# Kernel optimization log

Hardware: AMD Instinct MI355X
Metric: run time of the kernel (lower is better)

The kernel has to match this reference:

```python
import jax, jax.numpy as jnp
import numpy as np

N_NODES = 50000
N_EDGES = 625000
FEAT = 128
NEG_SLOPE = 0.2  # dgl GATConv default leaky_relu slope


def setup_inputs() -> dict:
    key = jax.random.key(0)
    ks = jax.random.split(key, 16)
    x = jax.random.normal(ks[0], (N_NODES, FEAT), dtype=jnp.float32)
    src = jax.random.randint(ks[1], (N_EDGES,), 0, N_NODES, dtype=jnp.int32)
    dst = jax.random.randint(ks[2], (N_EDGES,), 0, N_NODES, dtype=jnp.int32)
    s = 1.0 / np.sqrt(FEAT)
    d = {"x": x, "src": src, "dst": dst}
    for i in range(3):
        d[f"W{i+1}"] = jax.random.normal(ks[3 + 4 * i], (FEAT, FEAT), dtype=jnp.float32) * s
        d[f"al{i+1}"] = jax.random.normal(ks[4 + 4 * i], (FEAT,), dtype=jnp.float32) * s
        d[f"ar{i+1}"] = jax.random.normal(ks[5 + 4 * i], (FEAT,), dtype=jnp.float32) * s
        d[f"b{i+1}"] = jnp.zeros((FEAT,), dtype=jnp.float32)
    return d


def gat_layer(h_in, src, dst, W, al, ar, b):
    # dgl GATConv, num_heads=1: fc -> edge attention -> edge_softmax -> scatter
    h = h_in @ W                                   # [N, F]
    el = h @ al                                    # [N]
    er = h @ ar                                    # [N]
    e = jax.nn.leaky_relu(el[src] + er[dst], NEG_SLOPE)   # [E]
    # numerically stable edge softmax, grouped by destination node
    m = jax.ops.segment_max(e, dst, num_segments=N_NODES)  # [N]
    ex = jnp.exp(e - m[dst])
    denom = jax.ops.segment_sum(ex, dst, num_segments=N_NODES)
    alpha = ex / denom[dst]                        # [E]
    out = jax.ops.segment_sum(alpha[:, None] * h[src], dst, num_segments=N_NODES)
    return out + b


def reference(x, src, dst, W1, al1, ar1, b1, W2, al2, ar2, b2, W3, al3, ar3, b3):
    h = gat_layer(x, src, dst, W1, al1, ar1, b1)
    h = jax.nn.relu(h)
    h = gat_layer(h, src, dst, W2, al2, ar2, b2)
    h = jax.nn.relu(h)
    h = gat_layer(h, src, dst, W3, al3, ar3, b3)
    return h
```

## Files before the change

kernel.cpp:

```cpp
#include <hip/hip_runtime.h>
#include <hip/hip_fp16.h>

#define N_NODES 50000
#define N_EDGES 625000
#define FEAT 128
#define NEG_SLOPE 0.2f
#define NB_SCAN 196

typedef __attribute__((ext_vector_type(8))) short bf16x8;
typedef __attribute__((ext_vector_type(4))) float f32x4;

__device__ __forceinline__ unsigned short f2bf(float f) {
  unsigned u = __float_as_uint(f);
  u += 0x7fffu + ((u >> 16) & 1u);
  return (unsigned short)(u >> 16);
}
__device__ __forceinline__ float bf2f(unsigned short s) {
  return __uint_as_float(((unsigned)s) << 16);
}


__global__ __launch_bounds__(256) void prepzero_kernel(
    const float* __restrict__ W0, const float* __restrict__ W1, const float* __restrict__ W2,
    unsigned short* __restrict__ wfhi, unsigned short* __restrict__ wflo,
    int* __restrict__ cnt) {
  int bb = blockIdx.x;
  if (bb < 192) {
    int idx = bb * 256 + threadIdx.x;
    if (idx >= 3 * FEAT * FEAT) return;
    int l = idx >> 14, rem = idx & 16383;
    int e = rem & 7, lane = (rem >> 3) & 63, kb = (rem >> 9) & 3, ct = rem >> 11;
    int col = ct * 16 + (lane & 15);
    int k   = kb * 32 + (lane >> 4) * 8 + e;
    const float* W = (l == 0) ? W0 : ((l == 1) ? W1 : W2);
    float v = W[k * FEAT + col];
    unsigned short hi = f2bf(v);
    wfhi[idx] = hi;
    wflo[idx] = f2bf(v - bf2f(hi));
  } else {
    int i = (bb - 192) * 256 + threadIdx.x;
    if (i < N_NODES + 16) cnt[i] = 0;
  }
}


__global__ __launch_bounds__(256) void hist_kernel(const int* __restrict__ dst,
                                                   int* __restrict__ cnt) {
  int e = blockIdx.x * 256 + threadIdx.x;
  if (e < N_EDGES) atomicAdd(&cnt[dst[e]], 1);
}

__global__ __launch_bounds__(256) void scan_part_kernel(const int* __restrict__ cnt,
                                                        int* __restrict__ part) {
  __shared__ int s[256];
  int i = blockIdx.x * 256 + threadIdx.x;
  s[threadIdx.x] = (i < N_NODES) ? cnt[i] : 0;
  __syncthreads();
  for (int o = 128; o > 0; o >>= 1) {
    if (threadIdx.x < o) s[threadIdx.x] += s[threadIdx.x + o];
    __syncthreads();
  }
  if (threadIdx.x == 0) part[blockIdx.x] = s[0];
}

__global__ __launch_bounds__(256) void scan_top_kernel(int* __restrict__ part,
                                                       int* __restrict__ offs) {
  __shared__ int s[256];
  int tid = threadIdx.x;
  int v = (tid < NB_SCAN) ? part[tid] : 0;
  s[tid] = v;
  __syncthreads();
  for (int o = 1; o < 256; o <<= 1) {
    int t = (tid >= o) ? s[tid - o] : 0;
    __syncthreads();
    s[tid] += t;
    __syncthreads();
  }
  if (tid < NB_SCAN) part[tid] = s[tid] - v;
  if (tid == 255) offs[N_NODES] = s[255];
}

__global__ __launch_bounds__(256) void scan_down_kernel(int* __restrict__ cnt,
                                                        const int* __restrict__ part,
                                                        int* __restrict__ offs) {
  __shared__ int s[256];
  int tid = threadIdx.x;
  int i = blockIdx.x * 256 + tid;
  int v = (i < N_NODES) ? cnt[i] : 0;
  s[tid] = v;
  __syncthreads();
  for (int o = 1; o < 256; o <<= 1) {
    int t = (tid >= o) ? s[tid - o] : 0;
    __syncthreads();
    s[tid] += t;
    __syncthreads();
  }
  if (i < N_NODES) {
    int excl = s[tid] - v + part[blockIdx.x];
    offs[i] = excl;
    cnt[i] = excl;
  }
}

__global__ __launch_bounds__(256) void fill_kernel(const int* __restrict__ src,
                                                   const int* __restrict__ dst,
                                                   int* __restrict__ cursor,
                                                   int* __restrict__ ssrc) {
  int e = blockIdx.x * 256 + threadIdx.x;
  if (e < N_EDGES) {
    int pos = atomicAdd(&cursor[dst[e]], 1);
    ssrc[pos] = src[e];
  }
}


__global__ __launch_bounds__(256) void gemm_mfma_kernel(
    const float* __restrict__ inF, const __half* __restrict__ inH,
    const unsigned short* __restrict__ wfhi, const unsigned short* __restrict__ wflo,
    const float* __restrict__ al, const float* __restrict__ ar,
    __half* __restrict__ h, float* __restrict__ el, float* __restrict__ er,
    int fp16relu_in)
{
  __shared__ unsigned short wl[16384];
  __shared__ __half tile[64][132];
  const int tid = threadIdx.x;
  const int wave = tid >> 6, lane = tid & 63;
  const int lrow = lane & 15, lkb = lane >> 4;
  const int arow_i = blockIdx.x * 64 + wave * 16 + lrow;
  const bool avalid = arow_i < N_NODES;

#pragma unroll
  for (int q = 0; q < 8; ++q) {
    int idx = q * 256 + tid;
    int hilo = idx >> 10, r = idx & 1023, frag = r >> 6, word = r & 63;
    int ct = frag >> 1, kb = frag & 1;
    const uint4* s4 = (const uint4*)(hilo ? wflo : wfhi);
    uint4 v = s4[(ct * 4 + kb) * 64 + word];
    *(uint4*)&wl[((hilo * 16 + frag) << 9) + word * 8] = v;
  }

  bf16x8 ahi[4], alo[4];
#pragma unroll
  for (int kb = 0; kb < 4; ++kb) {
    float a[8];
    if (avalid) {
      if (fp16relu_in) {
        const unsigned short* aH = (const unsigned short*)inH + (size_t)arow_i * FEAT;
        uint4 rv = *(const uint4*)(aH + kb * 32 + lkb * 8);
        const __half2* hp = (const __half2*)&rv;
#pragma unroll
        for (int e2 = 0; e2 < 4; ++e2) {
          float2 f = __half22float2(hp[e2]);
          a[e2 * 2] = fmaxf(f.x, 0.f); a[e2 * 2 + 1] = fmaxf(f.y, 0.f);
        }
      } else {
        const float* arow = inF + (size_t)arow_i * FEAT;
        float4 v0 = *(const float4*)(arow + kb * 32 + lkb * 8);
        float4 v1 = *(const float4*)(arow + kb * 32 + lkb * 8 + 4);
        a[0] = v0.x; a[1] = v0.y; a[2] = v0.z; a[3] = v0.w;
        a[4] = v1.x; a[5] = v1.y; a[6] = v1.z; a[7] = v1.w;
      }
    } else {
#pragma unroll
      for (int e = 0; e < 8; ++e) a[e] = 0.f;
    }
#pragma unroll
    for (int e = 0; e < 8; ++e) {
      unsigned short hb = f2bf(a[e]);
      ahi[kb][e] = (short)hb;
      alo[kb][e] = (short)f2bf(a[e] - bf2f(hb));
    }
  }

  f32x4 acc[8];
#pragma unroll
  for (int ct = 0; ct < 8; ++ct)
#pragma unroll
    for (int r = 0; r < 4; ++r) acc[ct][r] = 0.f;

  __syncthreads();
#pragma unroll
  for (int ct = 0; ct < 8; ++ct) {
#pragma unroll
    for (int kb1 = 0; kb1 < 2; ++kb1) {
      bf16x8 bhi = *(const bf16x8*)&wl[((ct * 2 + kb1) << 9) + lane * 8];
      bf16x8 blo = *(const bf16x8*)&wl[((16 + ct * 2 + kb1) << 9) + lane * 8];
      acc[ct] = __builtin_amdgcn_mfma_f32_16x16x32_bf16(ahi[kb1], bhi, acc[ct], 0, 0, 0);
      acc[ct] = __builtin_amdgcn_mfma_f32_16x16x32_bf16(ahi[kb1], blo, acc[ct], 0, 0, 0);
      acc[ct] = __builtin_amdgcn_mfma_f32_16x16x32_bf16(alo[kb1], bhi, acc[ct], 0, 0, 0);
    }
  }
  __syncthreads();

#pragma unroll
  for (int q = 0; q < 8; ++q) {
    int idx = q * 256 + tid;
    int hilo = idx >> 10, r = idx & 1023, frag = r >> 6, word = r & 63;
    int ct = frag >> 1, kb = 2 + (frag & 1);
    const uint4* s4 = (const uint4*)(hilo ? wflo : wfhi);
    uint4 v = s4[(ct * 4 + kb) * 64 + word];
    *(uint4*)&wl[((hilo * 16 + frag) << 9) + word * 8] = v;
  }
  __syncthreads();
#pragma unroll
  for (int ct = 0; ct < 8; ++ct) {
#pragma unroll
    for (int kb1 = 0; kb1 < 2; ++kb1) {
      bf16x8 bhi = *(const bf16x8*)&wl[((ct * 2 + kb1) << 9) + lane * 8];
      bf16x8 blo = *(const bf16x8*)&wl[((16 + ct * 2 + kb1) << 9) + lane * 8];
      acc[ct] = __builtin_amdgcn_mfma_f32_16x16x32_bf16(ahi[2 + kb1], bhi, acc[ct], 0, 0, 0);
      acc[ct] = __builtin_amdgcn_mfma_f32_16x16x32_bf16(ahi[2 + kb1], blo, acc[ct], 0, 0, 0);
      acc[ct] = __builtin_amdgcn_mfma_f32_16x16x32_bf16(alo[2 + kb1], bhi, acc[ct], 0, 0, 0);
    }
  }

  float alv[8], arv[8];
#pragma unroll
  for (int ct = 0; ct < 8; ++ct) { alv[ct] = al[ct * 16 + lrow]; arv[ct] = ar[ct * 16 + lrow]; }

  const int lrow0 = wave * 16 + lkb * 4;
#pragma unroll
  for (int r = 0; r < 4; ++r) {
    float pel = 0.f, per_ = 0.f;
#pragma unroll
    for (int ct = 0; ct < 8; ++ct) {
      float v = acc[ct][r];
      tile[lrow0 + r][ct * 16 + lrow] = __float2half_rn(v);
      pel  = fmaf(v, alv[ct], pel);
      per_ = fmaf(v, arv[ct], per_);
    }
#pragma unroll
    for (int mask = 8; mask >= 1; mask >>= 1) {
      pel  += __shfl_xor(pel, mask);
      per_ += __shfl_xor(per_, mask);
    }
    int grow = blockIdx.x * 64 + lrow0 + r;
    if (grow < N_NODES && lrow == 0) { el[grow] = pel; er[grow] = per_; }
  }
  __syncthreads();

  const int row0g = blockIdx.x * 64;
#pragma unroll
  for (int it = 0; it < 4; ++it) {
    int idx = it * 256 + tid;
    int row = idx >> 4, c16 = idx & 15;
    int grow = row0g + row;
    if (grow < N_NODES) {
      uint4 v = *(const uint4*)&tile[row][c16 * 8];
      *((uint4*)(h + (size_t)grow * FEAT) + c16) = v;
    }
  }
}


__global__ __launch_bounds__(256) void agg_kernel(
    const __half* __restrict__ h, const float* __restrict__ el,
    const float* __restrict__ er, const int* __restrict__ offs,
    const int* __restrict__ ssrc, const float* __restrict__ bias,
    float* __restrict__ out32, __half* __restrict__ out16, int use16)
{
  const int wid = (blockIdx.x * 256 + threadIdx.x) >> 6;
  const int lane = threadIdx.x & 63;
  if (wid >= N_NODES) return;
  const int qg = lane >> 4;
  const int ql = lane & 15;

  const int beg = offs[wid], end = offs[wid + 1];
  const float erd = er[wid];
  const unsigned short* __restrict__ hu = (const unsigned short*)h;

  float acc[8];
#pragma unroll
  for (int f = 0; f < 8; ++f) acc[f] = 0.f;
  float denom = 0.f, m = -1e30f;

  for (int base = beg; base < end; base += 64) {
    const int n = min(64, end - base);

    int s = 0;
    float e = -1e30f;
    if (lane < n) {
      s = ssrc[base + lane];
      float t = el[s] + erd;
      e = t > 0.f ? t : NEG_SLOPE * t;
    }

    float cm = e;
#pragma unroll
    for (int mask = 32; mask > 0; mask >>= 1) cm = fmaxf(cm, __shfl_xor(cm, mask));
    if (cm > m) {
      float sc = __expf(m - cm);
#pragma unroll
      for (int f = 0; f < 8; ++f) acc[f] *= sc;
      denom *= sc;
      m = cm;
    }

    float ex = (lane < n) ? __expf(e - m) : 0.f;
    float ds = ex;
#pragma unroll
    for (int mask = 32; mask > 0; mask >>= 1) ds += __shfl_xor(ds, mask);
    denom += ds;

    for (int g = 0; g < n; g += 16) {
      uint4 raw[4];
      float w[4];
#pragma unroll
      for (int l = 0; l < 4; ++l) {
        int j = g + l * 4 + qg;
        int sj = __shfl(s, j);
        w[l] = __shfl(ex, j);
        raw[l] = *(const uint4*)(hu + (((size_t)sj) << 7) + (ql << 3));
      }
#pragma unroll
      for (int l = 0; l < 4; ++l) {
        float2 f0 = __half22float2(__builtin_bit_cast(__half2, raw[l].x));
        float2 f1 = __half22float2(__builtin_bit_cast(__half2, raw[l].y));
        float2 f2 = __half22float2(__builtin_bit_cast(__half2, raw[l].z));
        float2 f3 = __half22float2(__builtin_bit_cast(__half2, raw[l].w));
        acc[0] = fmaf(w[l], f0.x, acc[0]); acc[1] = fmaf(w[l], f0.y, acc[1]);
        acc[2] = fmaf(w[l], f1.x, acc[2]); acc[3] = fmaf(w[l], f1.y, acc[3]);
        acc[4] = fmaf(w[l], f2.x, acc[4]); acc[5] = fmaf(w[l], f2.y, acc[5]);
        acc[6] = fmaf(w[l], f3.x, acc[6]); acc[7] = fmaf(w[l], f3.y, acc[7]);
      }
    }
  }

#pragma unroll
  for (int f = 0; f < 8; ++f) {
    acc[f] += __shfl_xor(acc[f], 16);
    acc[f] += __shfl_xor(acc[f], 32);
  }

  float inv = denom > 0.f ? 1.f / denom : 0.f;
  if (use16) {
    if (qg == 0) {
      float4 b0 = ((const float4*)bias)[ql * 2];
      float4 b1 = ((const float4*)bias)[ql * 2 + 1];
      __half2 o[4];
      o[0] = __floats2half2_rn(fmaf(acc[0], inv, b0.x), fmaf(acc[1], inv, b0.y));
      o[1] = __floats2half2_rn(fmaf(acc[2], inv, b0.z), fmaf(acc[3], inv, b0.w));
      o[2] = __floats2half2_rn(fmaf(acc[4], inv, b1.x), fmaf(acc[5], inv, b1.y));
      o[3] = __floats2half2_rn(fmaf(acc[6], inv, b1.z), fmaf(acc[7], inv, b1.w));
      ((uint4*)(out16 + ((size_t)wid << 7)))[ql] = *(const uint4*)o;
    }
  } else {
    if (qg < 2) {
      float4 bv = ((const float4*)bias)[ql * 2 + qg];
      float4 o;
      o.x = fmaf(acc[qg * 4 + 0], inv, bv.x);
      o.y = fmaf(acc[qg * 4 + 1], inv, bv.y);
      o.z = fmaf(acc[qg * 4 + 2], inv, bv.z);
      o.w = fmaf(acc[qg * 4 + 3], inv, bv.w);
      ((float4*)out32)[((size_t)wid << 5) + ql * 2 + qg] = o;
    }
  }
}


extern "C" void kernel_launch(void* const* d_in, const int* in_sizes, int n_in,
                              void* d_out, int out_size, void* d_ws, size_t ws_size,
                              hipStream_t stream) {
  const float* x  = (const float*)d_in[0];
  const int* src  = (const int*)d_in[1];
  const int* dst  = (const int*)d_in[2];
  const float* W[3]  = {(const float*)d_in[3],  (const float*)d_in[7],  (const float*)d_in[11]};
  const float* al[3] = {(const float*)d_in[4],  (const float*)d_in[8],  (const float*)d_in[12]};
  const float* ar[3] = {(const float*)d_in[5],  (const float*)d_in[9],  (const float*)d_in[13]};
  const float* b[3]  = {(const float*)d_in[6],  (const float*)d_in[10], (const float*)d_in[14]};

  __half* hH    = (__half*)d_ws;
  __half* out16 = hH + 6400000;
  float*  el    = (float*)(out16 + 6400000);
  float*  er    = el + 50016;
  int*    cnt   = (int*)(er + 50016);
  int*    offs  = cnt + 50016;
  int*    part  = offs + 50016;
  int*    ssrc  = part + 256;
  unsigned short* wfhi = (unsigned short*)(ssrc + 625000);
  unsigned short* wflo = wfhi + 3 * FEAT * FEAT;

  prepzero_kernel<<<392, 256, 0, stream>>>(W[0], W[1], W[2], wfhi, wflo, cnt);
  hist_kernel<<<(N_EDGES + 255) / 256, 256, 0, stream>>>(dst, cnt);
  scan_part_kernel<<<NB_SCAN, 256, 0, stream>>>(cnt, part);
  scan_top_kernel<<<1, 256, 0, stream>>>(part, offs);
  scan_down_kernel<<<NB_SCAN, 256, 0, stream>>>(cnt, part, offs);
  fill_kernel<<<(N_EDGES + 255) / 256, 256, 0, stream>>>(src, dst, cnt, ssrc);

  const int gemm_grid = (N_NODES + 63) / 64;
  const int agg_grid  = (N_NODES + 3) / 4;
  float* outf = (float*)d_out;

  for (int l = 0; l < 3; ++l) {
    gemm_mfma_kernel<<<gemm_grid, 256, 0, stream>>>(
        (l == 0) ? x : nullptr, (l == 0) ? nullptr : out16,
        wfhi + l * FEAT * FEAT, wflo + l * FEAT * FEAT,
        al[l], ar[l], hH, el, er, l > 0 ? 1 : 0);
    agg_kernel<<<agg_grid, 256, 0, stream>>>(
        hH, el, er, offs, ssrc, b[l], outf, out16, l < 2 ? 1 : 0);
  }
}
```

Measured before the change: 234.1 us.

## Assign one destination node per 16-lane quarter-wave and drop softmax max pass

The aggregation kernel now maps four destination nodes onto each 64-lane wave, one per 16-lane group, instead of one node per wave. This suits the average in-degree of about 12 and avoids leaving most lanes idle. The online-max rescaling is gone: edge logits are exponentiated directly and the denominator is reduced within each 16-lane group, which removes several cross-lane reductions per chunk. The trade-off is that very large attention logits could overflow without max subtraction, and quarters with different degrees now diverge inside a wave.

```diff
diff --git a/kernel.cpp b/kernel.cpp
--- a/kernel.cpp
+++ b/kernel.cpp
@@ -259,101 +259,84 @@
     const int* __restrict__ ssrc, const float* __restrict__ bias,
     float* __restrict__ out32, __half* __restrict__ out16, int use16)
 {
-  const int wid = (blockIdx.x * 256 + threadIdx.x) >> 6;
-  const int lane = threadIdx.x & 63;
-  if (wid >= N_NODES) return;
-  const int qg = lane >> 4;
-  const int ql = lane & 15;
-
-  const int beg = offs[wid], end = offs[wid + 1];
-  const float erd = er[wid];
+  const int tid = threadIdx.x;
+  const int lane = tid & 63;
+  const int qg = lane >> 4, ql = lane & 15;
+  const int waveg = (blockIdx.x * 256 + tid) >> 6;
+  const int node = waveg * 4 + qg;
+  if (node >= N_NODES) return;
+
+  const int beg = offs[node], end = offs[node + 1];
+  const float erd = er[node];
   const unsigned short* __restrict__ hu = (const unsigned short*)h;
+  const int qbase = qg * 16;
 
   float acc[8];
 #pragma unroll
   for (int f = 0; f < 8; ++f) acc[f] = 0.f;
-  float denom = 0.f, m = -1e30f;
-
-  for (int base = beg; base < end; base += 64) {
-    const int n = min(64, end - base);
-
+  float ds = 0.f;
+
+  for (int base = beg; base < end; base += 16) {
+    const int idx = base + ql;
+    const bool v = idx < end;
     int s = 0;
-    float e = -1e30f;
-    if (lane < n) {
-      s = ssrc[base + lane];
+    float ex = 0.f;
+    if (v) s = ssrc[idx];
+    if (v) {
       float t = el[s] + erd;
-      e = t > 0.f ? t : NEG_SLOPE * t;
-    }
-
-    float cm = e;
-#pragma unroll
-    for (int mask = 32; mask > 0; mask >>= 1) cm = fmaxf(cm, __shfl_xor(cm, mask));
-    if (cm > m) {
-      float sc = __expf(m - cm);
-#pragma unroll
-      for (int f = 0; f < 8; ++f) acc[f] *= sc;
-      denom *= sc;
-      m = cm;
-    }
-
-    float ex = (lane < n) ? __expf(e - m) : 0.f;
-    float ds = ex;
-#pragma unroll
-    for (int mask = 32; mask > 0; mask >>= 1) ds += __shfl_xor(ds, mask);
-    denom += ds;
-
-    for (int g = 0; g < n; g += 16) {
-      uint4 raw[4];
-      float w[4];
+      t = t > 0.f ? t : NEG_SLOPE * t;
+      ex = __expf(t);
+    }
+    ds += ex;
+
+    const int ne = min(16, end - base);
+    for (int j = 0; j < ne; j += 4) {
+      int   s0 = __shfl(s,  qbase + j),     s1 = __shfl(s,  qbase + j + 1);
+      int   s2 = __shfl(s,  qbase + j + 2), s3 = __shfl(s,  qbase + j + 3);
+      float w0 = __shfl(ex, qbase + j),     w1 = __shfl(ex, qbase + j + 1);
+      float w2 = __shfl(ex, qbase + j + 2), w3 = __shfl(ex, qbase + j + 3);
+      uint4 r0 = *(const uint4*)(hu + (((size_t)s0) << 7) + (ql << 3));
+      uint4 r1 = *(const uint4*)(hu + (((size_t)s1) << 7) + (ql << 3));
+      uint4 r2 = *(const uint4*)(hu + (((size_t)s2) << 7) + (ql << 3));
+      uint4 r3 = *(const uint4*)(hu + (((size_t)s3) << 7) + (ql << 3));
 #pragma unroll
       for (int l = 0; l < 4; ++l) {
-        int j = g + l * 4 + qg;
-        int sj = __shfl(s, j);
-        w[l] = __shfl(ex, j);
-        raw[l] = *(const uint4*)(hu + (((size_t)sj) << 7) + (ql << 3));
+        const uint4& rr = (l == 0) ? r0 : (l == 1) ? r1 : (l == 2) ? r2 : r3;
+        const float  ww = (l == 0) ? w0 : (l == 1) ? w1 : (l == 2) ? w2 : w3;
+        float2 f0 = __half22float2(__builtin_bit_cast(__half2, rr.x));
+        float2 f1 = __half22float2(__builtin_bit_cast(__half2, rr.y));
+        float2 f2 = __half22float2(__builtin_bit_cast(__half2, rr.z));
+        float2 f3 = __half22float2(__builtin_bit_cast(__half2, rr.w));
+        acc[0] = fmaf(ww, f0.x, acc[0]); acc[1] = fmaf(ww, f0.y, acc[1]);
+        acc[2] = fmaf(ww, f1.x, acc[2]); acc[3] = fmaf(ww, f1.y, acc[3]);
+        acc[4] = fmaf(ww, f2.x, acc[4]); acc[5] = fmaf(ww, f2.y, acc[5]);
+        acc[6] = fmaf(ww, f3.x, acc[6]); acc[7] = fmaf(ww, f3.y, acc[7]);
       }
-#pragma unroll
-      for (int l = 0; l < 4; ++l) {
-        float2 f0 = __half22float2(__builtin_bit_cast(__half2, raw[l].x));
-        float2 f1 = __half22float2(__builtin_bit_cast(__half2, raw[l].y));
-        float2 f2 = __half22float2(__builtin_bit_cast(__half2, raw[l].z));
-        float2 f3 = __half22float2(__builtin_bit_cast(__half2, raw[l].w));
-        acc[0] = fmaf(w[l], f0.x, acc[0]); acc[1] = fmaf(w[l], f0.y, acc[1]);
-        acc[2] = fmaf(w[l], f1.x, acc[2]); acc[3] = fmaf(w[l], f1.y, acc[3]);
-        acc[4] = fmaf(w[l], f2.x, acc[4]); acc[5] = fmaf(w[l], f2.y, acc[5]);
-        acc[6] = fmaf(w[l], f3.x, acc[6]); acc[7] = fmaf(w[l], f3.y, acc[7]);
-      }
-    }
-  }
-
-#pragma unroll
-  for (int f = 0; f < 8; ++f) {
-    acc[f] += __shfl_xor(acc[f], 16);
-    acc[f] += __shfl_xor(acc[f], 32);
-  }
-
-  float inv = denom > 0.f ? 1.f / denom : 0.f;
+    }
+  }
+
+#pragma unroll
+  for (int mask = 8; mask >= 1; mask >>= 1) ds += __shfl_xor(ds, mask);
+  const float inv = ds > 0.f ? 1.f / ds : 0.f;
+
+  float4 b0 = ((const float4*)bias)[ql * 2];
+  float4 b1 = ((const float4*)bias)[ql * 2 + 1];
+  float o0 = fmaf(acc[0], inv, b0.x), o1 = fmaf(acc[1], inv, b0.y);
+  float o2 = fmaf(acc[2], inv, b0.z), o3 = fmaf(acc[3], inv, b0.w);
+  float o4 = fmaf(acc[4], inv, b1.x), o5 = fmaf(acc[5], inv, b1.y);
+  float o6 = fmaf(acc[6], inv, b1.z), o7 = fmaf(acc[7], inv, b1.w);
+
   if (use16) {
-    if (qg == 0) {
-      float4 b0 = ((const float4*)bias)[ql * 2];
-      float4 b1 = ((const float4*)bias)[ql * 2 + 1];
-      __half2 o[4];
-      o[0] = __floats2half2_rn(fmaf(acc[0], inv, b0.x), fmaf(acc[1], inv, b0.y));
-      o[1] = __floats2half2_rn(fmaf(acc[2], inv, b0.z), fmaf(acc[3], inv, b0.w));
-      o[2] = __floats2half2_rn(fmaf(acc[4], inv, b1.x), fmaf(acc[5], inv, b1.y));
-      o[3] = __floats2half2_rn(fmaf(acc[6], inv, b1.z), fmaf(acc[7], inv, b1.w));
-      ((uint4*)(out16 + ((size_t)wid << 7)))[ql] = *(const uint4*)o;
-    }
+    __half2 o[4];
+    o[0] = __floats2half2_rn(o0, o1);
+    o[1] = __floats2half2_rn(o2, o3);
+    o[2] = __floats2half2_rn(o4, o5);
+    o[3] = __floats2half2_rn(o6, o7);
+    ((uint4*)(out16 + ((size_t)node << 7)))[ql] = *(const uint4*)o;
   } else {
-    if (qg < 2) {
-      float4 bv = ((const float4*)bias)[ql * 2 + qg];
-      float4 o;
-      o.x = fmaf(acc[qg * 4 + 0], inv, bv.x);
-      o.y = fmaf(acc[qg * 4 + 1], inv, bv.y);
-      o.z = fmaf(acc[qg * 4 + 2], inv, bv.z);
-      o.w = fmaf(acc[qg * 4 + 3], inv, bv.w);
-      ((float4*)out32)[((size_t)wid << 5) + ql * 2 + qg] = o;
-    }
+    float4* op = (float4*)(out32 + ((size_t)node << 7)) + ql * 2;
+    op[0] = make_float4(o0, o1, o2, o3);
+    op[1] = make_float4(o4, o5, o6, o7);
   }
 }
 
@@ -388,7 +371,7 @@
   fill_kernel<<<(N_EDGES + 255) / 256, 256, 0, stream>>>(src, dst, cnt, ssrc);
 
   const int gemm_grid = (N_NODES + 63) / 64;
-  const int agg_grid  = (N_NODES + 3) / 4;
+  const int agg_grid  = (N_NODES + 15) / 16;
   float* outf = (float*)d_out;
 
   for (int l = 0; l < 3; ++l) {
```

Result: faster. 209.7 us (median of 2 runs) (-10.4%).
